# Kernel tuning notes

Measured on AMD Instinct MI355X. Metric: run time of the kernel, lower is better.

## Reference

```python
import jax, jax.numpy as jnp
import numpy as np


def setup_inputs() -> dict:
    key = jax.random.key(0)
    qkv = jax.random.normal(key, (8, 1536, 2048), dtype=jnp.float32)
    return {"qkv": qkv, "n_heads": 8}


def reference(qkv, n_heads):
    # qkv: [N, H*3*C, T] -> output [N, H*C, T]
    bs, width, length = qkv.shape
    assert width % (3 * n_heads) == 0
    ch = width // (3 * n_heads)
    qkv_r = qkv.reshape(bs * n_heads, 3 * ch, length)
    q, k, v = qkv_r[:, :ch], qkv_r[:, ch:2 * ch], qkv_r[:, 2 * ch:]
    scale = 1.0 / np.sqrt(np.sqrt(ch))  # applied to both q and k
    # [B, T, S] scores
    weight = jnp.einsum('bct,bcs->bts', q * scale, k * scale)
    weight = jax.nn.softmax(weight.astype(jnp.float32), axis=-1).astype(weight.dtype)
    a = jnp.einsum('bts,bcs->bct', weight, v)
    return a.reshape(bs, n_heads * ch, length)
```

## Files before the change

kernel.cpp:

```cpp
#include <hip/hip_runtime.h>


typedef __bf16 bf16;
typedef __bf16 bf16x4 __attribute__((ext_vector_type(4)));
typedef __bf16 bf16x8 __attribute__((ext_vector_type(8)));
typedef float  f32x4  __attribute__((ext_vector_type(4)));
typedef float  f32x16 __attribute__((ext_vector_type(16)));
typedef unsigned int u32;

#define NLEN 2048
#define DCH  64
#define HSTR (NLEN * DCH * 2)
#define WS_K (16u * 1024u * 1024u)
#define WS_V (32u * 1024u * 1024u)
#define WS_NEED (48u * 1024u * 1024u)
#define PSCALE 0.42466119f

__device__ __forceinline__ int swzK(int row, int cb) {
    return row * 128 + ((((cb >> 4) ^ row) & 7) << 4) + (cb & 15);
}
__device__ __forceinline__ int swzO(int row, int cb) {
    int g = cb >> 4;
    g = (g & ~7) | ((g ^ row) & 7);
    return row * 512 + (g << 4) + (cb & 15);
}

__device__ __forceinline__ void gload16(const char* g, char* l) {
    __builtin_amdgcn_global_load_lds((const __attribute__((address_space(1))) void*)g,
                                     (__attribute__((address_space(3))) void*)l, 16, 0, 0);
}

__global__ __launch_bounds__(256)
void prep(const float* __restrict__ qkv, char* __restrict__ ws)
{
    const int tid  = threadIdx.x;
    const int pb   = blockIdx.x;
    const int head = blockIdx.y;
    const int type = blockIdx.z;

    const float* src = qkv + (size_t)head * (3 * DCH) * NLEN + (size_t)type * DCH * NLEN;
    char* dst = ws + (type == 0 ? 0u : (type == 1 ? WS_K : WS_V))
                   + (size_t)head * HSTR + (size_t)pb * 8192;

    if (type < 2) {
        __shared__ float T[64][65];
        #pragma unroll
        for (int p = 0; p < 4; ++p) {
            int idx = tid + p * 256;
            int c = idx >> 4, q4 = idx & 15;
            float4 f = *(const float4*)(src + (size_t)c * NLEN + pb * 64 + q4 * 4);
            T[q4 * 4 + 0][c] = f.x * PSCALE;
            T[q4 * 4 + 1][c] = f.y * PSCALE;
            T[q4 * 4 + 2][c] = f.z * PSCALE;
            T[q4 * 4 + 3][c] = f.w * PSCALE;
        }
        __syncthreads();
        #pragma unroll
        for (int p = 0; p < 2; ++p) {
            int gidx = tid + p * 256;
            int s = gidx >> 3, G = gidx & 7;
            if (type == 0) {
                int c0 = (G ^ (s & 7)) * 8;
                bf16 tmp[8];
                #pragma unroll
                for (int j = 0; j < 8; ++j) tmp[j] = (bf16)T[s][c0 + j];
                *(bf16x8*)(dst + s * 128 + G * 16) = *(bf16x8*)tmp;
            } else {
                const int kc = G >> 1, hi = G & 1;
                bf16 tmp[8];
                #pragma unroll
                for (int j = 0; j < 8; ++j) tmp[j] = (bf16)T[s][G * 8 + j];
                *(bf16x8*)(dst + kc * 2048 + ((s >> 5) & 1) * 1024 + hi * 512
                               + (s & 31) * 16) = *(bf16x8*)tmp;
            }
        }
    } else {
        const int c = tid >> 2, m = tid & 3;
        const float* sp = src + (size_t)c * NLEN + pb * 64 + m * 16;
        float f[16];
        #pragma unroll
        for (int j = 0; j < 4; ++j) *(f32x4*)(f + 4 * j) = *(const f32x4*)(sp + 4 * j);
        #pragma unroll
        for (int gl = 0; gl < 2; ++gl) {
            bf16 tmp[8];
            #pragma unroll
            for (int j = 0; j < 8; ++j) tmp[j] = (bf16)f[gl * 8 + j];
            *(bf16x8*)(dst + m * 2048 + ((c >> 5) & 1) * 1024 + gl * 512
                           + (c & 31) * 16) = *(bf16x8*)tmp;
        }
    }
}

__device__ __forceinline__ void expcvt(f32x16& slo, f32x16& shi, float& l, bf16x8 pa[4])
{
    float a = 0.f, b = 0.f, c = 0.f, d = 0.f;
    #pragma unroll
    for (int r = 0; r < 16; r += 4) {
        slo[r+0] = __builtin_amdgcn_exp2f(slo[r+0]); a += slo[r+0];
        slo[r+1] = __builtin_amdgcn_exp2f(slo[r+1]); b += slo[r+1];
        slo[r+2] = __builtin_amdgcn_exp2f(slo[r+2]); c += slo[r+2];
        slo[r+3] = __builtin_amdgcn_exp2f(slo[r+3]); d += slo[r+3];
    }
    #pragma unroll
    for (int r = 0; r < 16; r += 4) {
        shi[r+0] = __builtin_amdgcn_exp2f(shi[r+0]); a += shi[r+0];
        shi[r+1] = __builtin_amdgcn_exp2f(shi[r+1]); b += shi[r+1];
        shi[r+2] = __builtin_amdgcn_exp2f(shi[r+2]); c += shi[r+2];
        shi[r+3] = __builtin_amdgcn_exp2f(shi[r+3]); d += shi[r+3];
    }
    l += (a + b) + (c + d);
    #pragma unroll
    for (int ks = 0; ks < 4; ++ks) {
        const f32x16& pp = (ks < 2) ? slo : shi;
        const int rb = (ks & 1) * 8;
        u32 X, X2, Y, Y2;
        asm("v_cvt_pk_bf16_f32 %0, %1, %2" : "=v"(X)  : "v"(pp[rb + 0]), "v"(pp[rb + 1]));
        asm("v_cvt_pk_bf16_f32 %0, %1, %2" : "=v"(X2) : "v"(pp[rb + 2]), "v"(pp[rb + 3]));
        asm("v_cvt_pk_bf16_f32 %0, %1, %2" : "=v"(Y)  : "v"(pp[rb + 4]), "v"(pp[rb + 5]));
        asm("v_cvt_pk_bf16_f32 %0, %1, %2" : "=v"(Y2) : "v"(pp[rb + 6]), "v"(pp[rb + 7]));
        asm("v_permlane32_swap_b32 %0, %1" : "+v"(X),  "+v"(Y));
        asm("v_permlane32_swap_b32 %0, %1" : "+v"(X2), "+v"(Y2));
        u32 wds[4] = {X, X2, Y, Y2};
        pa[ks] = *(bf16x8*)wds;
    }
}

__global__ __launch_bounds__(256, 2)
void attn_main(const char* __restrict__ ws, float* __restrict__ out)
{
    const int tid  = threadIdx.x;
    const int lane = tid & 63;
    const int w    = tid >> 6;
    const int hi   = lane >> 5;
    const int ll5  = lane & 31;

    const int bid  = blockIdx.x;
    const int head = (bid & 7) * 8 + ((bid >> 3) & 7);
    const int tblk = bid >> 6;
    const int t0   = tblk * 256;
    const int sbase = ((bid >> 3) & 1) * 16;

    const char* Qb = ws + (size_t)head * HSTR + (size_t)t0 * 128;
    const char* Kb = ws + WS_K + (size_t)head * HSTR;
    const char* Vb = ws + WS_V + (size_t)head * HSTR;

    __shared__ __align__(16) char lds[32768];

    #pragma unroll
    for (int i = 0; i < 8; ++i)
        gload16(Qb + tid * 16 + i * 4096, lds + tid * 16 + i * 4096);
    asm volatile("s_waitcnt vmcnt(0)");
    __syncthreads();

    bf16x8 qf0[4], qf1[4];
    #pragma unroll
    for (int kc = 0; kc < 4; ++kc) {
        qf0[kc] = *(const bf16x8*)(lds + swzK(w * 64 + ll5,      kc * 32 + hi * 16));
        qf1[kc] = *(const bf16x8*)(lds + swzK(w * 64 + 32 + ll5, kc * 32 + hi * 16));
    }

    const int voff = hi * 512 + ll5 * 16;

    bf16x8 kf0[4], kf1[4];
    {
        const char* Kt = Kb + (size_t)sbase * 8192 + voff;
        #pragma unroll
        for (int kc = 0; kc < 4; ++kc) {
            kf0[kc] = *(const bf16x8*)(Kt + kc * 2048);
            kf1[kc] = *(const bf16x8*)(Kt + kc * 2048 + 1024);
        }
    }

    f32x16 o00 = {}, o01 = {}, o10 = {}, o11 = {};
    float l0 = 0.f, l1 = 0.f;

    #pragma unroll 1
    for (int i = 0; i < 32; ++i) {
        const int ti = (i + sbase) & 31;

        bf16x8 vf0[4], vf1[4];
        {
            const char* Vt = Vb + (size_t)ti * 8192 + voff;
            #pragma unroll
            for (int ks = 0; ks < 4; ++ks) {
                vf0[ks] = *(const bf16x8*)(Vt + ks * 2048);
                vf1[ks] = *(const bf16x8*)(Vt + ks * 2048 + 1024);
            }
        }

        f32x16 sa = {}, sb = {};
        __builtin_amdgcn_s_setprio(1);
        #pragma unroll
        for (int kc = 0; kc < 4; ++kc) {
            sa = __builtin_amdgcn_mfma_f32_32x32x16_bf16(kf0[kc], qf0[kc], sa, 0, 0, 0);
            sb = __builtin_amdgcn_mfma_f32_32x32x16_bf16(kf1[kc], qf0[kc], sb, 0, 0, 0);
        }
        __builtin_amdgcn_s_setprio(0);
        bf16x8 pa0[4];
        expcvt(sa, sb, l0, pa0);

        f32x16 sc = {}, sd = {};
        __builtin_amdgcn_s_setprio(1);
        #pragma unroll
        for (int kc = 0; kc < 4; ++kc) {
            sc = __builtin_amdgcn_mfma_f32_32x32x16_bf16(kf0[kc], qf1[kc], sc, 0, 0, 0);
            sd = __builtin_amdgcn_mfma_f32_32x32x16_bf16(kf1[kc], qf1[kc], sd, 0, 0, 0);
        }
        __builtin_amdgcn_s_setprio(0);

        if (i != 31) {
            const char* Kt = Kb + (size_t)(((i + 1 + sbase) & 31)) * 8192 + voff;
            #pragma unroll
            for (int kc = 0; kc < 4; ++kc) {
                kf0[kc] = *(const bf16x8*)(Kt + kc * 2048);
                kf1[kc] = *(const bf16x8*)(Kt + kc * 2048 + 1024);
            }
        }

        bf16x8 pa1[4];
        expcvt(sc, sd, l1, pa1);

        __builtin_amdgcn_s_setprio(1);
        #pragma unroll
        for (int ks = 0; ks < 4; ++ks) {
            o00 = __builtin_amdgcn_mfma_f32_32x32x16_bf16(pa0[ks], vf0[ks], o00, 0, 0, 0);
            o01 = __builtin_amdgcn_mfma_f32_32x32x16_bf16(pa0[ks], vf1[ks], o01, 0, 0, 0);
            o10 = __builtin_amdgcn_mfma_f32_32x32x16_bf16(pa1[ks], vf0[ks], o10, 0, 0, 0);
            o11 = __builtin_amdgcn_mfma_f32_32x32x16_bf16(pa1[ks], vf1[ks], o11, 0, 0, 0);
        }
        __builtin_amdgcn_s_setprio(0);
    }

    const float lf0 = l0 + __shfl_xor(l0, 32);
    const float lf1 = l1 + __shfl_xor(l1, 32);
    const float li0 = 1.0f / lf0;
    const float li1 = 1.0f / lf1;
    float a0[16], a1[16];
    #pragma unroll
    for (int r = 0; r < 16; ++r) {
        const int src = (r & 3) + 8 * (r >> 2) + 4 * hi;
        a0[r] = __shfl(li0, src);
        a1[r] = __shfl(li1, src);
    }
    #pragma unroll
    for (int r = 0; r < 16; ++r) {
        o00[r] *= a0[r]; o01[r] *= a0[r];
        o10[r] *= a1[r]; o11[r] *= a1[r];
    }

    float* op = out + (size_t)head * DCH * NLEN + t0;
    float* Of = (float*)lds;

    #pragma unroll
    for (int p = 0; p < 2; ++p) {
        __syncthreads();
        if ((w >> 1) == p) {
            const int wl = w & 1;
            #pragma unroll
            for (int th = 0; th < 2; ++th) {
                const f32x16& v0 = th ? o10 : o00;
                const f32x16& v1 = th ? o11 : o01;
                #pragma unroll
                for (int j = 0; j < 4; ++j) {
                    const int tb = wl * 64 + th * 32 + 8 * j + 4 * hi;
                    f32x4 u0, u1;
                    #pragma unroll
                    for (int r = 0; r < 4; ++r) { u0[r] = v0[4 * j + r]; u1[r] = v1[4 * j + r]; }
                    *(f32x4*)((char*)Of + swzO(ll5,      tb * 4)) = u0;
                    *(f32x4*)((char*)Of + swzO(32 + ll5, tb * 4)) = u1;
                }
            }
        }
        __syncthreads();
        #pragma unroll
        for (int ch = 0; ch < 8; ++ch) {
            const int idx = tid + ch * 256;
            const int c = idx >> 5, tq = idx & 31;
            f32x4 v = *(const f32x4*)((char*)Of + swzO(c, tq * 16));
            *(float4*)(op + (size_t)c * NLEN + p * 128 + tq * 4) = *(float4*)&v;
        }
    }
}

#define QSCALE_FB 0.35355339059327373f
__global__ __launch_bounds__(512, 2)
void attn_fwd(const float* __restrict__ qkv, float* __restrict__ out)
{
    const int tid  = threadIdx.x;
    const int lane = tid & 63;
    const int w    = tid >> 6;
    const int lg   = lane >> 4;
    const int ll   = lane & 15;
    const int tblk = blockIdx.x;
    const int head = blockIdx.y;
    const int t0   = tblk * 128;

    const float* qp = qkv + (size_t)head * (3 * DCH) * NLEN;
    const float* kp = qp + (size_t)DCH * NLEN;
    const float* vp = kp + (size_t)DCH * NLEN;

    __shared__ __align__(16) char lds[48 * 1024];
    char* Qs = lds;
    char* Ks = lds + 16 * 1024;
    char* Vs = lds + 24 * 1024;
    char* Ps = lds + 32 * 1024 + w * 2048;

    {
        const int G = tid >> 6;
        #pragma unroll
        for (int it = 0; it < 2; ++it) {
            const int t = (tid & 63) + it * 64;
            const float* src = qp + (size_t)(G * 8) * NLEN + t0 + t;
            bf16 tmp[8];
            #pragma unroll
            for (int j = 0; j < 8; ++j) tmp[j] = (bf16)(src[(size_t)j * NLEN] * QSCALE_FB);
            *(bf16x8*)(Qs + swzK(t, G * 16)) = *(bf16x8*)tmp;
        }
    }
    __syncthreads();
    bf16x8 qf[2];
    #pragma unroll
    for (int kk = 0; kk < 2; ++kk)
        qf[kk] = *(const bf16x8*)(Qs + swzK(w * 16 + ll, kk * 64 + lg * 16));

    f32x4 o[4] = {};
    float m_r = -3.0e38f, l_r = 0.f;

    for (int sb = 0; sb < NLEN / 64; ++sb) {
        const int s0 = sb * 64;
        __syncthreads();
        {
            const int s = tid & 63, G = tid >> 6;
            const float* src = kp + (size_t)(G * 8) * NLEN + s0 + s;
            bf16 tmp[8];
            #pragma unroll
            for (int j = 0; j < 8; ++j) tmp[j] = (bf16)(src[(size_t)j * NLEN] * QSCALE_FB);
            *(bf16x8*)(Ks + swzK(s, G * 16)) = *(bf16x8*)tmp;
        }
        {
            const int c = tid >> 3, s8 = tid & 7;
            const float* src = vp + (size_t)c * NLEN + s0 + s8 * 8;
            const float4 f0 = *(const float4*)src;
            const float4 f1 = *(const float4*)(src + 4);
            bf16 tmp[8] = {(bf16)f0.x, (bf16)f0.y, (bf16)f0.z, (bf16)f0.w,
                           (bf16)f1.x, (bf16)f1.y, (bf16)f1.z, (bf16)f1.w};
            *(bf16x8*)(Vs + swzK(c, s8 * 16)) = *(bf16x8*)tmp;
        }
        __syncthreads();

        f32x4 sf[4] = {};
        #pragma unroll
        for (int kk = 0; kk < 2; ++kk)
            #pragma unroll
            for (int fs = 0; fs < 4; ++fs) {
                bf16x8 a = *(const bf16x8*)(Ks + swzK(fs * 16 + ll, kk * 64 + lg * 16));
                sf[fs] = __builtin_amdgcn_mfma_f32_16x16x32_bf16(a, qf[kk], sf[fs], 0, 0, 0);
            }

        float mx;
        {
            f32x4 m4 = sf[0];
            #pragma unroll
            for (int fs = 1; fs < 4; ++fs) {
                m4[0] = fmaxf(m4[0], sf[fs][0]); m4[1] = fmaxf(m4[1], sf[fs][1]);
                m4[2] = fmaxf(m4[2], sf[fs][2]); m4[3] = fmaxf(m4[3], sf[fs][3]);
            }
            mx = fmaxf(fmaxf(m4[0], m4[1]), fmaxf(m4[2], m4[3]));
        }
        mx = fmaxf(mx, __shfl_xor(mx, 16));
        mx = fmaxf(mx, __shfl_xor(mx, 32));
        const float mnew = fmaxf(m_r, mx);
        const float corr = exp2f((m_r - mnew) * 1.4426950408889634f);
        m_r = mnew;
        const float cm = mnew * 1.4426950408889634f;

        float psum = 0.f;
        #pragma unroll
        for (int fs = 0; fs < 4; ++fs) {
            bf16x4 pw;
            #pragma unroll
            for (int r = 0; r < 4; ++r) {
                float p = exp2f(fmaf(sf[fs][r], 1.4426950408889634f, -cm));
                psum += p;
                pw[r] = (bf16)p;
            }
            *(bf16x4*)(Ps + swzK(ll, 32 * fs + 8 * lg)) = pw;
        }
        psum += __shfl_xor(psum, 16);
        psum += __shfl_xor(psum, 32);
        l_r = l_r * corr + psum;

        float corr4[4];
        #pragma unroll
        for (int r = 0; r < 4; ++r) corr4[r] = __shfl(corr, 4 * lg + r);
        #pragma unroll
        for (int cf = 0; cf < 4; ++cf)
            #pragma unroll
            for (int r = 0; r < 4; ++r) o[cf][r] *= corr4[r];

        #pragma unroll
        for (int kk = 0; kk < 2; ++kk) {
            bf16x8 pa = *(const bf16x8*)(Ps + swzK(ll, kk * 64 + lg * 16));
            #pragma unroll
            for (int cf = 0; cf < 4; ++cf) {
                bf16x8 b = *(const bf16x8*)(Vs + swzK(cf * 16 + ll, kk * 64 + lg * 16));
                o[cf] = __builtin_amdgcn_mfma_f32_16x16x32_bf16(pa, b, o[cf], 0, 0, 0);
            }
        }
    }

    __syncthreads();
    const float linv = 1.0f / l_r;
    float linv4[4];
    #pragma unroll
    for (int r = 0; r < 4; ++r) linv4[r] = __shfl(linv, 4 * lg + r);
    float* Of = (float*)lds;
    #pragma unroll
    for (int cf = 0; cf < 4; ++cf) {
        f32x4 ov;
        #pragma unroll
        for (int r = 0; r < 4; ++r) ov[r] = o[cf][r] * linv4[r];
        *(f32x4*)((char*)Of + swzO(cf * 16 + ll, (w * 16 + 4 * lg) * 4)) = ov;
    }
    __syncthreads();
    float* op = out + (size_t)head * DCH * NLEN + t0;
    #pragma unroll
    for (int it = 0; it < 4; ++it) {
        const int idx = tid + it * 512;
        const int c = idx >> 5, tq = idx & 31;
        f32x4 v = *(const f32x4*)((char*)Of + swzO(c, tq * 16));
        *(float4*)(op + (size_t)c * NLEN + tq * 4) = *(float4*)&v;
    }
}

extern "C" void kernel_launch(void* const* d_in, const int* in_sizes, int n_in,
                              void* d_out, int out_size, void* d_ws, size_t ws_size,
                              hipStream_t stream)
{
    const float* qkv = (const float*)d_in[0];
    float* out = (float*)d_out;
    if (ws_size >= (size_t)WS_NEED) {
        char* ws = (char*)d_ws;
        prep<<<dim3(32, 64, 3), 256, 0, stream>>>(qkv, ws);
        attn_main<<<dim3(512), 256, 0, stream>>>(ws, out);
    } else {
        attn_fwd<<<dim3(16, 64), 512, 0, stream>>>(qkv, out);
    }
}
```

Baseline: 102.6 us.

## Halve attn_main block to 128 threads and double grid to 1024 blocks

```diff
diff --git a/kernel.cpp b/kernel.cpp
--- a/kernel.cpp
+++ b/kernel.cpp
@@ -125,7 +125,7 @@
     }
 }
 
-__global__ __launch_bounds__(256, 2)
+__global__ __launch_bounds__(128, 2)
 void attn_main(const char* __restrict__ ws, float* __restrict__ out)
 {
     const int tid  = threadIdx.x;
@@ -135,10 +135,10 @@
     const int ll5  = lane & 31;
 
     const int bid  = blockIdx.x;
-    const int head = (bid & 7) * 8 + ((bid >> 3) & 7);
-    const int tblk = bid >> 6;
-    const int t0   = tblk * 256;
-    const int sbase = ((bid >> 3) & 1) * 16;
+    const int j    = bid >> 3;
+    const int head = (bid & 7) * 8 + (j & 7);
+    const int tblk = j >> 3;
+    const int t0   = tblk * 128;
 
     const char* Qb = ws + (size_t)head * HSTR + (size_t)t0 * 128;
     const char* Kb = ws + WS_K + (size_t)head * HSTR;
@@ -148,7 +148,7 @@
 
     #pragma unroll
     for (int i = 0; i < 8; ++i)
-        gload16(Qb + tid * 16 + i * 4096, lds + tid * 16 + i * 4096);
+        gload16(Qb + tid * 16 + i * 2048, lds + tid * 16 + i * 2048);
     asm volatile("s_waitcnt vmcnt(0)");
     __syncthreads();
 
@@ -162,13 +162,10 @@
     const int voff = hi * 512 + ll5 * 16;
 
     bf16x8 kf0[4], kf1[4];
-    {
-        const char* Kt = Kb + (size_t)sbase * 8192 + voff;
-        #pragma unroll
-        for (int kc = 0; kc < 4; ++kc) {
-            kf0[kc] = *(const bf16x8*)(Kt + kc * 2048);
-            kf1[kc] = *(const bf16x8*)(Kt + kc * 2048 + 1024);
-        }
+    #pragma unroll
+    for (int kc = 0; kc < 4; ++kc) {
+        kf0[kc] = *(const bf16x8*)(Kb + voff + kc * 2048);
+        kf1[kc] = *(const bf16x8*)(Kb + voff + kc * 2048 + 1024);
     }
 
     f32x16 o00 = {}, o01 = {}, o10 = {}, o11 = {};
@@ -176,11 +173,9 @@
 
     #pragma unroll 1
     for (int i = 0; i < 32; ++i) {
-        const int ti = (i + sbase) & 31;
-
         bf16x8 vf0[4], vf1[4];
         {
-            const char* Vt = Vb + (size_t)ti * 8192 + voff;
+            const char* Vt = Vb + (size_t)i * 8192 + voff;
             #pragma unroll
             for (int ks = 0; ks < 4; ++ks) {
                 vf0[ks] = *(const bf16x8*)(Vt + ks * 2048);
@@ -189,27 +184,23 @@
         }
 
         f32x16 sa = {}, sb = {};
-        __builtin_amdgcn_s_setprio(1);
         #pragma unroll
         for (int kc = 0; kc < 4; ++kc) {
             sa = __builtin_amdgcn_mfma_f32_32x32x16_bf16(kf0[kc], qf0[kc], sa, 0, 0, 0);
             sb = __builtin_amdgcn_mfma_f32_32x32x16_bf16(kf1[kc], qf0[kc], sb, 0, 0, 0);
         }
-        __builtin_amdgcn_s_setprio(0);
         bf16x8 pa0[4];
         expcvt(sa, sb, l0, pa0);
 
         f32x16 sc = {}, sd = {};
-        __builtin_amdgcn_s_setprio(1);
         #pragma unroll
         for (int kc = 0; kc < 4; ++kc) {
             sc = __builtin_amdgcn_mfma_f32_32x32x16_bf16(kf0[kc], qf1[kc], sc, 0, 0, 0);
             sd = __builtin_amdgcn_mfma_f32_32x32x16_bf16(kf1[kc], qf1[kc], sd, 0, 0, 0);
         }
-        __builtin_amdgcn_s_setprio(0);
 
         if (i != 31) {
-            const char* Kt = Kb + (size_t)(((i + 1 + sbase) & 31)) * 8192 + voff;
+            const char* Kt = Kb + (size_t)(i + 1) * 8192 + voff;
             #pragma unroll
             for (int kc = 0; kc < 4; ++kc) {
                 kf0[kc] = *(const bf16x8*)(Kt + kc * 2048);
@@ -220,7 +211,6 @@
         bf16x8 pa1[4];
         expcvt(sc, sd, l1, pa1);
 
-        __builtin_amdgcn_s_setprio(1);
         #pragma unroll
         for (int ks = 0; ks < 4; ++ks) {
             o00 = __builtin_amdgcn_mfma_f32_32x32x16_bf16(pa0[ks], vf0[ks], o00, 0, 0, 0);
@@ -228,7 +218,6 @@
             o10 = __builtin_amdgcn_mfma_f32_32x32x16_bf16(pa1[ks], vf0[ks], o10, 0, 0, 0);
             o11 = __builtin_amdgcn_mfma_f32_32x32x16_bf16(pa1[ks], vf1[ks], o11, 0, 0, 0);
         }
-        __builtin_amdgcn_s_setprio(0);
     }
 
     const float lf0 = l0 + __shfl_xor(l0, 32);
@@ -248,37 +237,31 @@
         o10[r] *= a1[r]; o11[r] *= a1[r];
     }
 
+    __syncthreads();
+    float* Of = (float*)lds;
+    #pragma unroll
+    for (int th = 0; th < 2; ++th) {
+        const f32x16& v0 = th ? o10 : o00;
+        const f32x16& v1 = th ? o11 : o01;
+        #pragma unroll
+        for (int jj = 0; jj < 4; ++jj) {
+            const int tb = w * 64 + th * 32 + 8 * jj + 4 * hi;
+            f32x4 u0, u1;
+            #pragma unroll
+            for (int r = 0; r < 4; ++r) { u0[r] = v0[4 * jj + r]; u1[r] = v1[4 * jj + r]; }
+            *(f32x4*)((char*)Of + swzO(ll5,      tb * 4)) = u0;
+            *(f32x4*)((char*)Of + swzO(32 + ll5, tb * 4)) = u1;
+        }
+    }
+    __syncthreads();
+
     float* op = out + (size_t)head * DCH * NLEN + t0;
-    float* Of = (float*)lds;
-
-    #pragma unroll
-    for (int p = 0; p < 2; ++p) {
-        __syncthreads();
-        if ((w >> 1) == p) {
-            const int wl = w & 1;
-            #pragma unroll
-            for (int th = 0; th < 2; ++th) {
-                const f32x16& v0 = th ? o10 : o00;
-                const f32x16& v1 = th ? o11 : o01;
-                #pragma unroll
-                for (int j = 0; j < 4; ++j) {
-                    const int tb = wl * 64 + th * 32 + 8 * j + 4 * hi;
-                    f32x4 u0, u1;
-                    #pragma unroll
-                    for (int r = 0; r < 4; ++r) { u0[r] = v0[4 * j + r]; u1[r] = v1[4 * j + r]; }
-                    *(f32x4*)((char*)Of + swzO(ll5,      tb * 4)) = u0;
-                    *(f32x4*)((char*)Of + swzO(32 + ll5, tb * 4)) = u1;
-                }
-            }
-        }
-        __syncthreads();
-        #pragma unroll
-        for (int ch = 0; ch < 8; ++ch) {
-            const int idx = tid + ch * 256;
-            const int c = idx >> 5, tq = idx & 31;
-            f32x4 v = *(const f32x4*)((char*)Of + swzO(c, tq * 16));
-            *(float4*)(op + (size_t)c * NLEN + p * 128 + tq * 4) = *(float4*)&v;
-        }
+    #pragma unroll
+    for (int ch = 0; ch < 16; ++ch) {
+        const int idx = tid + ch * 128;
+        const int c = idx >> 5, tq = idx & 31;
+        f32x4 v = *(const f32x4*)((char*)Of + swzO(c, tq * 16));
+        *(float4*)(op + (size_t)c * NLEN + tq * 4) = *(float4*)&v;
     }
 }
 
@@ -442,7 +425,7 @@
     if (ws_size >= (size_t)WS_NEED) {
         char* ws = (char*)d_ws;
         prep<<<dim3(32, 64, 3), 256, 0, stream>>>(qkv, ws);
-        attn_main<<<dim3(512), 256, 0, stream>>>(ws, out);
+        attn_main<<<dim3(1024), 128, 0, stream>>>(ws, out);
     } else {
         attn_fwd<<<dim3(16, 64), 512, 0, stream>>>(qkv, out);
     }
```

Result: no change. 100.8 us (-1.7%).
